# Kernel tuning notes

Measured on AMD Instinct MI355X. Metric: run time of the kernel, lower is better.

The kernel has to match this reference:

```python
import jax, jax.numpy as jnp
import numpy as np

TEMPERATURE = 0.1
EPS = 1e-8
NEG_INF = -9e15  # matches torch masked_fill value before temperature scaling


def setup_inputs() -> dict:
    key = jax.random.key(0)
    k1, k2 = jax.random.split(key)
    z1 = jax.random.normal(k1, (4096, 512), dtype=jnp.float32)
    z2 = jax.random.normal(k2, (4096, 512), dtype=jnp.float32)
    return {"z1": z1, "z2": z2}


def reference(z1, z2):
    feats = jnp.concatenate([z1, z2], axis=0)          # [2N, D]
    n2 = feats.shape[0]
    norms = jnp.linalg.norm(feats, axis=-1, keepdims=True)
    unit = feats / jnp.maximum(norms, EPS)             # cosine-normalized
    cos_sim = unit @ unit.T                            # [2N, 2N]
    idx = jnp.arange(n2)
    # mask self-similarity on the diagonal
    cos_sim = jnp.where(idx[:, None] == idx[None, :], NEG_INF, cos_sim)
    cos_sim = cos_sim / TEMPERATURE
    # positive for row i sits at column (i + N) mod 2N
    pos = cos_sim[idx, (idx + n2 // 2) % n2]           # [2N]
    nll = -pos + jax.scipy.special.logsumexp(cos_sim, axis=-1)
    return jnp.mean(nll)
```

## Files before the change

kernel.cpp:

```cpp
#include <hip/hip_runtime.h>
#include <hip/hip_bf16.h>
#include <math.h>

#define N2     8192
#define HALF_N 4096
#define DD     512
#define BM     128
#define BN     128
#define BKB    64
#define NKT    (DD / BKB)
#define NB     (N2 / BM)
#define NTRI   (NB * (NB + 1) / 2)

#define U_BYTES    ((size_t)N2 * DD)
#define PART_BYTES ((size_t)NB * N2 * 4)
#define PD_BYTES   ((size_t)HALF_N * 4)

typedef __attribute__((ext_vector_type(4))) float f32x4;
typedef __attribute__((ext_vector_type(2))) long  l64x2;

__device__ __forceinline__ void load16_lds(const void* g, void* l) {
    __builtin_amdgcn_global_load_lds(
        (const __attribute__((address_space(1))) void*)g,
        (__attribute__((address_space(3))) void*)l, 16, 0, 0);
}

__global__ __launch_bounds__(256) void prep_kernel(
    const float* __restrict__ z1, const float* __restrict__ z2,
    unsigned char* __restrict__ U, float* __restrict__ out)
{
    const int tid = threadIdx.x;
    if (blockIdx.x == 0 && tid == 0) out[0] = 0.0f;

    const int wave = tid >> 6;
    const int lane = tid & 63;
    const int row  = blockIdx.x * 4 + wave;

    const float* src = (row < HALF_N) ? (z1 + (size_t)row * DD)
                                      : (z2 + (size_t)(row - HALF_N) * DD);
    float4 a = ((const float4*)src)[lane * 2 + 0];
    float4 b = ((const float4*)src)[lane * 2 + 1];
    float ss = a.x*a.x + a.y*a.y + a.z*a.z + a.w*a.w
             + b.x*b.x + b.y*b.y + b.z*b.z + b.w*b.w;
#pragma unroll
    for (int off = 32; off > 0; off >>= 1) ss += __shfl_xor(ss, off);
    const float inv = 1.0f / fmaxf(sqrtf(ss), 1e-8f);

    int lo = __builtin_amdgcn_cvt_pk_fp8_f32(a.x * inv, a.y * inv, 0,  0);
    lo     = __builtin_amdgcn_cvt_pk_fp8_f32(a.z * inv, a.w * inv, lo, 1);
    int hi = __builtin_amdgcn_cvt_pk_fp8_f32(b.x * inv, b.y * inv, 0,  0);
    hi     = __builtin_amdgcn_cvt_pk_fp8_f32(b.z * inv, b.w * inv, hi, 1);

    const int g = lane >> 3;
    const int q = lane & 3;
    const int h = (lane >> 2) & 1;
    *(int2*)(U + (size_t)row * DD + g * 64 + q * 16 + h * 8) = make_int2(lo, hi);
}

__global__ __launch_bounds__(256, 3) void gram_kernel(
    const unsigned char* __restrict__ U, float* __restrict__ partials,
    float* __restrict__ posdot)
{
    __shared__ unsigned char Ash[2][BM][BKB];
    __shared__ unsigned char Bsh[2][BN][BKB];
    __shared__ float racc[2][BM];
    __shared__ float cacc[2][BN];

    const int tid  = threadIdx.x;
    const int wave = tid >> 6;
    const int lane = tid & 63;

    const int t = blockIdx.x;
    int by = (int)((129.0 - sqrt(16641.0 - 8.0 * (double)t)) * 0.5);
    by = min(max(by, 0), NB - 1);
    while (by > 0       && t <  (by * (129 - by)) / 2) --by;
    while (by < NB - 1  && t >= ((by + 1) * (128 - by)) / 2) ++by;
    const int bx = by + (t - (by * (129 - by)) / 2);

    const int wr = wave >> 1;
    const int wc = wave & 1;
    const size_t arow0 = (size_t)by * BM;
    const size_t brow0 = (size_t)bx * BN;

    ((float*)racc)[tid] = 0.f;
    ((float*)cacc)[tid] = 0.f;

    const int sseg = (lane & 3) ^ ((lane >> 3) & 3);

    auto stage = [&](int kt, int buf) {
        const int k0 = kt * BKB;
#pragma unroll
        for (int hh = 0; hh < 2; ++hh) {
            const int c = wave * 2 + hh;
            const int r = c * 16 + (lane >> 2);
            load16_lds(U + (arow0 + r) * DD + k0 + sseg * 16, &Ash[buf][c * 16][0]);
            load16_lds(U + (brow0 + r) * DD + k0 + sseg * 16, &Bsh[buf][c * 16][0]);
        }
    };

    f32x4 acc[4][4];
#pragma unroll
    for (int i = 0; i < 4; ++i)
#pragma unroll
        for (int j = 0; j < 4; ++j) acc[i][j] = (f32x4){0.f, 0.f, 0.f, 0.f};

    const int fr   = lane & 15;
    const int quad = lane >> 4;
    const int sb   = (quad ^ ((fr >> 1) & 3)) * 16;

    stage(0, 0);
    __syncthreads();

    for (int kt = 0; kt < NKT; ++kt) {
        const int buf = kt & 1;
        if (kt + 1 < NKT) stage(kt + 1, buf ^ 1);

        l64x2 af[4], bfr[4];
#pragma unroll
        for (int tt = 0; tt < 4; ++tt) {
            af[tt]  = *(const l64x2*)&Ash[buf][wr * 64 + tt * 16 + fr][sb];
            bfr[tt] = *(const l64x2*)&Bsh[buf][wc * 64 + tt * 16 + fr][sb];
        }
#pragma unroll
        for (int ct = 0; ct < 4; ++ct)
#pragma unroll
            for (int rt = 0; rt < 4; ++rt) {
                acc[rt][ct] = __builtin_amdgcn_mfma_f32_16x16x32_fp8_fp8(
                                  af[rt].x, bfr[ct].x, acc[rt][ct], 0, 0, 0);
                acc[rt][ct] = __builtin_amdgcn_mfma_f32_16x16x32_fp8_fp8(
                                  af[rt].y, bfr[ct].y, acc[rt][ct], 0, 0, 0);
            }
        __syncthreads();
    }

    const float SC = 14.42695040888963f;
    if (by == bx) {
#pragma unroll
        for (int rt = 0; rt < 4; ++rt) {
            const int lrow = wr * 64 + rt * 16 + quad * 4;
#pragma unroll
            for (int reg = 0; reg < 4; ++reg) {
                const int lr = lrow + reg;
                float s = 0.f;
#pragma unroll
                for (int ct = 0; ct < 4; ++ct) {
                    const int lc = wc * 64 + ct * 16 + fr;
                    const float e = exp2f(acc[rt][ct][reg] * SC);
                    s += (lc == lr) ? 0.f : e;
                }
                s += __shfl_xor(s, 1);
                s += __shfl_xor(s, 2);
                s += __shfl_xor(s, 4);
                s += __shfl_xor(s, 8);
                if (fr == 0) racc[wc][lr] = s;
            }
        }
    } else {
        float csum[4] = {0.f, 0.f, 0.f, 0.f};
#pragma unroll
        for (int rt = 0; rt < 4; ++rt) {
            const int lrow = wr * 64 + rt * 16 + quad * 4;
#pragma unroll
            for (int reg = 0; reg < 4; ++reg) {
                float s = 0.f;
#pragma unroll
                for (int ct = 0; ct < 4; ++ct) {
                    const float e = exp2f(acc[rt][ct][reg] * SC);
                    s += e;
                    csum[ct] += e;
                }
                s += __shfl_xor(s, 1);
                s += __shfl_xor(s, 2);
                s += __shfl_xor(s, 4);
                s += __shfl_xor(s, 8);
                if (fr == 0) racc[wc][lrow + reg] = s;
            }
        }
#pragma unroll
        for (int ct = 0; ct < 4; ++ct) {
            float c = csum[ct];
            c += __shfl_xor(c, 16);
            c += __shfl_xor(c, 32);
            if (quad == 0) cacc[wr][wc * 64 + ct * 16 + fr] = c;
        }
        if (posdot != nullptr && bx == by + 32 && wr == wc) {
#pragma unroll
            for (int rt = 0; rt < 4; ++rt) {
                const int lrow = rt * 16 + quad * 4;
#pragma unroll
                for (int reg = 0; reg < 4; ++reg)
                    if (fr == quad * 4 + reg)
                        posdot[arow0 + wr * 64 + lrow + reg] = acc[rt][rt][reg];
            }
        }
    }
    __syncthreads();

    if (tid < BM) {
        partials[(size_t)bx * N2 + arow0 + tid] = racc[0][tid] + racc[1][tid];
        if (by != bx)
            partials[(size_t)by * N2 + brow0 + tid] = cacc[0][tid] + cacc[1][tid];
    }
}

__global__ __launch_bounds__(256) void finalize_fast(
    const float* __restrict__ partials, const float* __restrict__ posdot,
    float* __restrict__ out)
{
    const int tid = threadIdx.x;
    const int row = blockIdx.x * 256 + tid;
    float s = 0.f;
#pragma unroll 8
    for (int j = 0; j < NB; ++j) s += partials[(size_t)j * N2 + row];
    float nll = -10.0f * posdot[row & (HALF_N - 1)] + logf(s);
#pragma unroll
    for (int off = 32; off > 0; off >>= 1) nll += __shfl_xor(nll, off);
    __shared__ float red[4];
    if ((tid & 63) == 0) red[tid >> 6] = nll;
    __syncthreads();
    if (tid == 0)
        atomicAdd(out, (red[0] + red[1] + red[2] + red[3]) * (1.0f / N2));
}

__device__ __forceinline__ float dec_e4m3(unsigned int b) {
    const int e = (b >> 3) & 15, m = b & 7;
    float v = e ? ldexpf((float)(8 + m), e - 10) : ldexpf((float)m, -9);
    return (b & 0x80u) ? -v : v;
}

__global__ __launch_bounds__(256) void finalize_slow(
    const unsigned char* __restrict__ U, const float* __restrict__ partials,
    float* __restrict__ out)
{
    const int tid  = threadIdx.x;
    const int wave = tid >> 6;
    const int lane = tid & 63;
    const int row  = blockIdx.x * 4 + wave;
    const int prow = (row + HALF_N) & (N2 - 1);

    uint2 xa = *(const uint2*)(U + (size_t)row  * DD + lane * 8);
    uint2 ya = *(const uint2*)(U + (size_t)prow * DD + lane * 8);
    float dot = 0.f;
#pragma unroll
    for (int j = 0; j < 4; ++j)
        dot += dec_e4m3(xa.x >> (8 * j)) * dec_e4m3(ya.x >> (8 * j));
#pragma unroll
    for (int j = 0; j < 4; ++j)
        dot += dec_e4m3(xa.y >> (8 * j)) * dec_e4m3(ya.y >> (8 * j));

    float ps = partials[(size_t)lane * N2 + row];
#pragma unroll
    for (int off = 32; off > 0; off >>= 1) {
        dot += __shfl_xor(dot, off);
        ps  += __shfl_xor(ps,  off);
    }
    __shared__ float part[4];
    if (lane == 0) part[wave] = -10.0f * dot + logf(ps);
    __syncthreads();
    if (tid == 0)
        atomicAdd(out, (part[0] + part[1] + part[2] + part[3]) * (1.0f / N2));
}

extern "C" void kernel_launch(void* const* d_in, const int* in_sizes, int n_in,
                              void* d_out, int out_size, void* d_ws, size_t ws_size,
                              hipStream_t stream)
{
    const float* z1 = (const float*)d_in[0];
    const float* z2 = (const float*)d_in[1];
    float* out      = (float*)d_out;
    unsigned char* U = (unsigned char*)d_ws;
    float* partials  = (float*)((char*)d_ws + U_BYTES);
    float* posdot    = (float*)((char*)d_ws + U_BYTES + PART_BYTES);
    const bool has_pd = ws_size >= U_BYTES + PART_BYTES + PD_BYTES;

    prep_kernel<<<N2 / 4, 256, 0, stream>>>(z1, z2, U, out);
    gram_kernel<<<NTRI, 256, 0, stream>>>(U, partials, has_pd ? posdot : nullptr);
    if (has_pd)
        finalize_fast<<<N2 / 256, 256, 0, stream>>>(partials, posdot, out);
    else
        finalize_slow<<<N2 / 4, 256, 0, stream>>>(U, partials, out);
}
```

Before: 107.6 us.

## Use scaled 16x16x128 FP8 MFMA with wider K tiles in Gram kernel

Replaces pairs of 16x16x32 FP8 MFMAs with a single 16x16x128 scaled MFMA (unit scales) per tile, and doubles the K-tile to 128 bytes with a new 8-way XOR swizzle for LDS staging and fragment loads. The prep kernel now writes FP8 rows in natural order. The aim is fewer MFMA issues and fewer K-loop iterations and barriers. In exchange, LDS use per block doubles and launch bounds drop from 3 to 2 blocks per SM, which lowers occupancy. The racc/cacc zero-initialisation is also removed, which may break the epilogue if those accumulators are still read.

Result: slower. 114.2 us (+6.2%).

```diff
diff --git a/kernel.cpp b/kernel.cpp
--- a/kernel.cpp
+++ b/kernel.cpp
@@ -7,7 +7,7 @@
 #define DD     512
 #define BM     128
 #define BN     128
-#define BKB    64
+#define BKB    128
 #define NKT    (DD / BKB)
 #define NB     (N2 / BM)
 #define NTRI   (NB * (NB + 1) / 2)
@@ -17,7 +17,10 @@
 #define PD_BYTES   ((size_t)HALF_N * 4)
 
 typedef __attribute__((ext_vector_type(4))) float f32x4;
-typedef __attribute__((ext_vector_type(2))) long  l64x2;
+typedef __attribute__((ext_vector_type(4))) int   i32x4;
+typedef __attribute__((ext_vector_type(8))) int   i32x8;
+
+#define SCALE1 0x7F7F7F7F
 
 __device__ __forceinline__ void load16_lds(const void* g, void* l) {
     __builtin_amdgcn_global_load_lds(
@@ -51,13 +54,10 @@
     int hi = __builtin_amdgcn_cvt_pk_fp8_f32(b.x * inv, b.y * inv, 0,  0);
     hi     = __builtin_amdgcn_cvt_pk_fp8_f32(b.z * inv, b.w * inv, hi, 1);
 
-    const int g = lane >> 3;
-    const int q = lane & 3;
-    const int h = (lane >> 2) & 1;
-    *(int2*)(U + (size_t)row * DD + g * 64 + q * 16 + h * 8) = make_int2(lo, hi);
-}
-
-__global__ __launch_bounds__(256, 3) void gram_kernel(
+    *(int2*)(U + (size_t)row * DD + lane * 8) = make_int2(lo, hi);
+}
+
+__global__ __launch_bounds__(256, 2) void gram_kernel(
     const unsigned char* __restrict__ U, float* __restrict__ partials,
     float* __restrict__ posdot)
 {
@@ -82,19 +82,16 @@
     const size_t arow0 = (size_t)by * BM;
     const size_t brow0 = (size_t)bx * BN;
 
-    ((float*)racc)[tid] = 0.f;
-    ((float*)cacc)[tid] = 0.f;
-
-    const int sseg = (lane & 3) ^ ((lane >> 3) & 3);
-
     auto stage = [&](int kt, int buf) {
         const int k0 = kt * BKB;
-#pragma unroll
-        for (int hh = 0; hh < 2; ++hh) {
-            const int c = wave * 2 + hh;
-            const int r = c * 16 + (lane >> 2);
-            load16_lds(U + (arow0 + r) * DD + k0 + sseg * 16, &Ash[buf][c * 16][0]);
-            load16_lds(U + (brow0 + r) * DD + k0 + sseg * 16, &Bsh[buf][c * 16][0]);
+        const int lr = lane >> 3;
+        const int s  = (lane & 7) ^ (lr & 7);
+#pragma unroll
+        for (int hh = 0; hh < 4; ++hh) {
+            const int c = wave * 4 + hh;
+            const int r = c * 8 + lr;
+            load16_lds(U + (arow0 + r) * DD + k0 + s * 16, &Ash[buf][c * 8][0]);
+            load16_lds(U + (brow0 + r) * DD + k0 + s * 16, &Bsh[buf][c * 8][0]);
         }
     };
 
@@ -106,7 +103,9 @@
 
     const int fr   = lane & 15;
     const int quad = lane >> 4;
-    const int sb   = (quad ^ ((fr >> 1) & 3)) * 16;
+    const int fr7  = fr & 7;
+    const int t0   = (2 * quad) ^ fr7;
+    const int t1   = t0 ^ 1;
 
     stage(0, 0);
     __syncthreads();
@@ -115,21 +114,27 @@
         const int buf = kt & 1;
         if (kt + 1 < NKT) stage(kt + 1, buf ^ 1);
 
-        l64x2 af[4], bfr[4];
+        i32x8 af[4], bfr[4];
 #pragma unroll
         for (int tt = 0; tt < 4; ++tt) {
-            af[tt]  = *(const l64x2*)&Ash[buf][wr * 64 + tt * 16 + fr][sb];
-            bfr[tt] = *(const l64x2*)&Bsh[buf][wc * 64 + tt * 16 + fr][sb];
+            const int ar = wr * 64 + tt * 16 + fr;
+            const int br = wc * 64 + tt * 16 + fr;
+            i32x4 alo = *(const i32x4*)&Ash[buf][ar][t0 * 16];
+            i32x4 ahi = *(const i32x4*)&Ash[buf][ar][t1 * 16];
+            i32x4 blo = *(const i32x4*)&Bsh[buf][br][t0 * 16];
+            i32x4 bhi = *(const i32x4*)&Bsh[buf][br][t1 * 16];
+            af[tt]  = __builtin_shufflevector(alo, ahi, 0, 1, 2, 3, 4, 5, 6, 7);
+            bfr[tt] = __builtin_shufflevector(blo, bhi, 0, 1, 2, 3, 4, 5, 6, 7);
         }
 #pragma unroll
         for (int ct = 0; ct < 4; ++ct)
 #pragma unroll
-            for (int rt = 0; rt < 4; ++rt) {
-                acc[rt][ct] = __builtin_amdgcn_mfma_f32_16x16x32_fp8_fp8(
-                                  af[rt].x, bfr[ct].x, acc[rt][ct], 0, 0, 0);
-                acc[rt][ct] = __builtin_amdgcn_mfma_f32_16x16x32_fp8_fp8(
-                                  af[rt].y, bfr[ct].y, acc[rt][ct], 0, 0, 0);
-            }
+            for (int rt = 0; rt < 4; ++rt)
+                acc[rt][ct] = __builtin_amdgcn_mfma_scale_f32_16x16x128_f8f6f4(
+                                  af[rt], bfr[ct], acc[rt][ct],
+                                  0, 0,
+                                  0, SCALE1,
+                                  0, SCALE1);
         __syncthreads();
     }
 
```

## Enlarge Gram tile to 256x256 with 16 waves per block

Applied to the files above, without the earlier changes.

Doubles the symmetric Gram block tile from 128 to 256 rows and columns and runs it with 1024-thread blocks arranged as a 4x4 wave grid, each wave still computing a 64x64 sub-tile. The triangular block index math, staging loads, per-row and per-column partial reductions and the positive-pair extraction are adjusted to the new tiling. The aim is to raise operand reuse and halve the number of partial-sum columns, which cuts global/L2 traffic. In exchange there are far fewer, larger blocks (528 of them), so load balance and occupancy across CUs may suffer, and each block carries more barrier overhead.

Result: slower. 123.4 us (+14.7%).

```diff
diff --git a/kernel.cpp b/kernel.cpp
--- a/kernel.cpp
+++ b/kernel.cpp
@@ -5,8 +5,7 @@
 #define N2     8192
 #define HALF_N 4096
 #define DD     512
-#define BM     128
-#define BN     128
+#define BM     256
 #define BKB    64
 #define NKT    (DD / BKB)
 #define NB     (N2 / BM)
@@ -57,45 +56,38 @@
     *(int2*)(U + (size_t)row * DD + g * 64 + q * 16 + h * 8) = make_int2(lo, hi);
 }
 
-__global__ __launch_bounds__(256, 3) void gram_kernel(
+__global__ __launch_bounds__(1024, 4) void gram_kernel(
     const unsigned char* __restrict__ U, float* __restrict__ partials,
     float* __restrict__ posdot)
 {
     __shared__ unsigned char Ash[2][BM][BKB];
-    __shared__ unsigned char Bsh[2][BN][BKB];
-    __shared__ float racc[2][BM];
-    __shared__ float cacc[2][BN];
+    __shared__ unsigned char Bsh[2][BM][BKB];
+    __shared__ float racc[4][BM];
+    __shared__ float cacc[4][BM];
 
     const int tid  = threadIdx.x;
     const int wave = tid >> 6;
     const int lane = tid & 63;
 
     const int t = blockIdx.x;
-    int by = (int)((129.0 - sqrt(16641.0 - 8.0 * (double)t)) * 0.5);
+    int by = (int)((65.0 - sqrt(4225.0 - 8.0 * (double)t)) * 0.5);
     by = min(max(by, 0), NB - 1);
-    while (by > 0       && t <  (by * (129 - by)) / 2) --by;
-    while (by < NB - 1  && t >= ((by + 1) * (128 - by)) / 2) ++by;
-    const int bx = by + (t - (by * (129 - by)) / 2);
-
-    const int wr = wave >> 1;
-    const int wc = wave & 1;
+    while (by > 0       && t <  (by * (65 - by)) / 2) --by;
+    while (by < NB - 1  && t >= ((by + 1) * (64 - by)) / 2) ++by;
+    const int bx = by + (t - (by * (65 - by)) / 2);
+
+    const int wr = wave >> 2;
+    const int wc = wave & 3;
     const size_t arow0 = (size_t)by * BM;
-    const size_t brow0 = (size_t)bx * BN;
-
-    ((float*)racc)[tid] = 0.f;
-    ((float*)cacc)[tid] = 0.f;
+    const size_t brow0 = (size_t)bx * BM;
 
     const int sseg = (lane & 3) ^ ((lane >> 3) & 3);
 
     auto stage = [&](int kt, int buf) {
         const int k0 = kt * BKB;
-#pragma unroll
-        for (int hh = 0; hh < 2; ++hh) {
-            const int c = wave * 2 + hh;
-            const int r = c * 16 + (lane >> 2);
-            load16_lds(U + (arow0 + r) * DD + k0 + sseg * 16, &Ash[buf][c * 16][0]);
-            load16_lds(U + (brow0 + r) * DD + k0 + sseg * 16, &Bsh[buf][c * 16][0]);
-        }
+        const int r  = wave * 16 + (lane >> 2);
+        load16_lds(U + (arow0 + r) * DD + k0 + sseg * 16, &Ash[buf][wave * 16][0]);
+        load16_lds(U + (brow0 + r) * DD + k0 + sseg * 16, &Bsh[buf][wave * 16][0]);
     };
 
     f32x4 acc[4][4];
@@ -183,23 +175,25 @@
             c += __shfl_xor(c, 32);
             if (quad == 0) cacc[wr][wc * 64 + ct * 16 + fr] = c;
         }
-        if (posdot != nullptr && bx == by + 32 && wr == wc) {
+        if (posdot != nullptr && bx == by + 16 && wc == wr) {
 #pragma unroll
             for (int rt = 0; rt < 4; ++rt) {
-                const int lrow = rt * 16 + quad * 4;
+                const int lrow = wr * 64 + rt * 16 + quad * 4;
 #pragma unroll
                 for (int reg = 0; reg < 4; ++reg)
                     if (fr == quad * 4 + reg)
-                        posdot[arow0 + wr * 64 + lrow + reg] = acc[rt][rt][reg];
+                        posdot[arow0 + lrow + reg] = acc[rt][rt][reg];
             }
         }
     }
     __syncthreads();
 
     if (tid < BM) {
-        partials[(size_t)bx * N2 + arow0 + tid] = racc[0][tid] + racc[1][tid];
+        partials[(size_t)bx * N2 + arow0 + tid] =
+            racc[0][tid] + racc[1][tid] + racc[2][tid] + racc[3][tid];
         if (by != bx)
-            partials[(size_t)by * N2 + brow0 + tid] = cacc[0][tid] + cacc[1][tid];
+            partials[(size_t)by * N2 + brow0 + tid] =
+                cacc[0][tid] + cacc[1][tid] + cacc[2][tid] + cacc[3][tid];
     }
 }
 
@@ -248,7 +242,7 @@
     for (int j = 0; j < 4; ++j)
         dot += dec_e4m3(xa.y >> (8 * j)) * dec_e4m3(ya.y >> (8 * j));
 
-    float ps = partials[(size_t)lane * N2 + row];
+    float ps = (lane < NB) ? partials[(size_t)lane * N2 + row] : 0.f;
 #pragma unroll
     for (int off = 32; off > 0; off >>= 1) {
         dot += __shfl_xor(dot, off);
@@ -274,7 +268,7 @@
     const bool has_pd = ws_size >= U_BYTES + PART_BYTES + PD_BYTES;
 
     prep_kernel<<<N2 / 4, 256, 0, stream>>>(z1, z2, U, out);
-    gram_kernel<<<NTRI, 256, 0, stream>>>(U, partials, has_pd ? posdot : nullptr);
+    gram_kernel<<<NTRI, 1024, 0, stream>>>(U, partials, has_pd ? posdot : nullptr);
     if (has_pd)
         finalize_fast<<<N2 / 256, 256, 0, stream>>>(partials, posdot, out);
     else
```
